# Performance work log

Measured on AMD Instinct MI355X. Metric: run time of the kernel, lower is better.

The kernel has to match this reference:

```python
import jax, jax.numpy as jnp
import numpy as np
from jax import lax

B, T, I, H = 1024, 64, 1024, 1024
EPS = 1e-5


def setup_inputs() -> dict:
    key = jax.random.key(0)
    ks = jax.random.split(key, 12)
    k = 1.0 / np.sqrt(H)  # torch RNNCell init bound
    return {
        "ui": jax.random.randint(ks[0], (B, 8), 0, 10000),
        "uv": jax.random.uniform(ks[1], (B, 8), dtype=jnp.float32),
        "ai": jax.random.randint(ks[2], (B, 8), 0, 10000),
        "av": jax.random.normal(ks[3], (B, T, I), dtype=jnp.float32),
        "y": jax.random.uniform(ks[4], (B, 1), dtype=jnp.float32),
        "W_ih": jax.random.uniform(ks[5], (H, I), minval=-k, maxval=k, dtype=jnp.float32),
        "b_ih": jax.random.uniform(ks[6], (H,), minval=-k, maxval=k, dtype=jnp.float32),
        "W_hh": jax.random.uniform(ks[7], (H, H), minval=-k, maxval=k, dtype=jnp.float32),
        "b_hh": jax.random.uniform(ks[8], (H,), minval=-k, maxval=k, dtype=jnp.float32),
        "W_out": jax.random.uniform(ks[9], (1, H), minval=-k, maxval=k, dtype=jnp.float32),
        "b_out": jax.random.uniform(ks[10], (1,), minval=-k, maxval=k, dtype=jnp.float32),
    }


def reference(ui, uv, ai, av, y, W_ih, b_ih, W_hh, b_hh, W_out, b_out):
    # av: [B, T, I] -> [T, B, I] (matches av.permute([1,0,2]) in source)
    x = jnp.transpose(av, (1, 0, 2))
    h0 = jnp.zeros((av.shape[0], W_hh.shape[0]), dtype=av.dtype)

    def step(h, xt):
        # torch.nn.RNNCell: h' = tanh(x W_ih^T + b_ih + h W_hh^T + b_hh)
        h_new = jnp.tanh(xt @ W_ih.T + b_ih + h @ W_hh.T + b_hh)
        return h_new, None

    h, _ = lax.scan(step, h0, x)
    out = jax.nn.sigmoid(h @ W_out.T + b_out)  # [B, 1]

    # y_true_bool = 1 where y >= 1e-5 else 0
    y_bool = (y >= EPS).astype(out.dtype)
    # torch BCELoss (mean reduction); clamp log like torch does (min -100)
    log_p = jnp.maximum(jnp.log(out), -100.0)
    log_1mp = jnp.maximum(jnp.log1p(-out), -100.0)
    loss = -jnp.mean(y_bool * log_p + (1.0 - y_bool) * log_1mp)
    return loss, out
```

## Files before the change

kernel.cpp:

```cpp
#include <hip/hip_runtime.h>

typedef __attribute__((ext_vector_type(8))) short bf16x8;
typedef __attribute__((ext_vector_type(4))) float f32x4;

__device__ __forceinline__ short f2bf(float f) {
    union { float f; unsigned u; } v; v.f = f;
    unsigned r = v.u + 0x7fffu + ((v.u >> 16) & 1u);
    return (short)(r >> 16);
}
__device__ __forceinline__ float bf2f(short s) {
    union { unsigned u; float f; } v; v.u = ((unsigned)(unsigned short)s) << 16;
    return v.f;
}
__device__ __forceinline__ unsigned pack2(float x, float y) {
    return (unsigned)(unsigned short)f2bf(x) | ((unsigned)(unsigned short)f2bf(y) << 16);
}
__device__ __forceinline__ uint4 pack8(float4 a, float4 b) {
    return make_uint4(pack2(a.x, a.y), pack2(a.z, a.w), pack2(b.x, b.y), pack2(b.z, b.w));
}
__device__ __forceinline__ float tanh_fast(float x) {
    float e = __expf(2.f * x);
    return 1.f - 2.f / (e + 1.f);
}

__device__ __forceinline__ void gll16(const void* gp, void* lp) {
    __builtin_amdgcn_global_load_lds(
        (__attribute__((address_space(1))) void*)gp,
        (__attribute__((address_space(3))) void*)lp, 16, 0, 0);
}

__global__ __launch_bounds__(256) void pack_w(const float* __restrict__ src,
                                              short* __restrict__ dst) {
    int idx = (blockIdx.x * 256 + threadIdx.x) * 8;
    float4 f0 = ((const float4*)(src + idx))[0];
    float4 f1 = ((const float4*)(src + idx))[1];
    *(uint4*)(dst + idx) = pack8(f0, f1);
}

__global__ void prep_b(const float* __restrict__ b_ih, const float* __restrict__ b_hh,
                       float* __restrict__ bsum) {
    int n = threadIdx.x;
    bsum[n] = b_ih[n] + b_hh[n];
}

__global__ __launch_bounds__(256) void conv_av(const float* __restrict__ av,
                                               short* __restrict__ X) {
    size_t e = ((size_t)blockIdx.x * 256 + threadIdx.x) * 8;
    size_t row = e >> 10;
    int k = (int)(e & 1023);
    int b = (int)(row >> 6), t = (int)(row & 63);
    float4 f0 = *(const float4*)(av + e);
    float4 f1 = *(const float4*)(av + e + 4);
    *(uint4*)(X + ((size_t)t * 1024 + b) * 1024 + k) = pack8(f0, f1);
}

__global__ __launch_bounds__(256) void zgemm2(const short* __restrict__ X,
                                              const short* __restrict__ Wih,
                                              const float* __restrict__ bsum,
                                              short* __restrict__ Z) {
    __shared__ short smem[16384];
    short* As = smem;
    short* Bs = smem + 8192;

    const int tid = threadIdx.x, lane = tid & 63, wave = tid >> 6;
    const int wm = wave >> 1, wn = wave & 1;
    const int m0 = blockIdx.y * 128, n0 = blockIdx.x * 128;

    const int srow = wave * 32 + (lane >> 3);
    const int scol = (lane & 7) * 8;
    const short* asrc = X   + (size_t)(m0 + srow) * 1024 + scol;
    const short* bsrc = Wih + (size_t)(n0 + srow) * 1024 + scol;
    char* aldst = (char*)As + wave * 4096;
    char* bldst = (char*)Bs + wave * 4096;

    f32x4 acc[4][4];
    #pragma unroll
    for (int i = 0; i < 4; i++)
        #pragma unroll
        for (int j = 0; j < 4; j++) acc[i][j] = (f32x4)0.0f;

    const int r = lane & 15, q = lane >> 4;
    const int koff = q * 8;

    for (int kt = 0; kt < 16; ++kt) {
        const int kbase = kt * 64;
        #pragma unroll
        for (int i = 0; i < 4; i++) {
            gll16(asrc + kbase + i * 8192, aldst + i * 1024);
            gll16(bsrc + kbase + i * 8192, bldst + i * 1024);
        }
        __syncthreads();

        #pragma unroll
        for (int ks = 0; ks < 2; ++ks) {
            bf16x8 af[4], bfr[4];
            #pragma unroll
            for (int i = 0; i < 4; i++) {
                af[i]  = *(const bf16x8*)&As[(wm * 64 + i * 16 + r) * 64 + ks * 32 + koff];
                bfr[i] = *(const bf16x8*)&Bs[(wn * 64 + i * 16 + r) * 64 + ks * 32 + koff];
            }
            #pragma unroll
            for (int i = 0; i < 4; i++)
                #pragma unroll
                for (int j = 0; j < 4; j++)
                    acc[i][j] = __builtin_amdgcn_mfma_f32_16x16x32_bf16(af[i], bfr[j], acc[i][j], 0, 0, 0);
        }
        __syncthreads();
    }

    short* Csh = smem;
    #pragma unroll
    for (int j = 0; j < 4; j++) {
        int colc = wn * 64 + j * 16 + r;
        float bs = bsum[n0 + colc];
        int chunkc = colc >> 3, rem = colc & 7;
        #pragma unroll
        for (int i = 0; i < 4; i++) {
            int rowb = wm * 64 + i * 16 + q * 4;
            #pragma unroll
            for (int rr = 0; rr < 4; rr++) {
                int row = rowb + rr;
                int sc = ((chunkc ^ (row & 7)) << 3) | rem;
                Csh[row * 128 + sc] = f2bf(acc[i][j][rr] + bs);
            }
        }
    }
    __syncthreads();
    #pragma unroll
    for (int p = 0; p < 8; p++) {
        int row = p * 16 + (tid >> 4);
        int chunk = tid & 15;
        int rc = chunk ^ (row & 7);
        uint4 v = *(const uint4*)&Csh[row * 128 + rc * 8];
        *(uint4*)(Z + (size_t)(m0 + row) * 1024 + n0 + chunk * 8) = v;
    }
}

#define ZLDK 72

__global__ __launch_bounds__(256) void zgemm(const float* __restrict__ av,
                                             const short* __restrict__ Wih,
                                             const float* __restrict__ bsum,
                                             short* __restrict__ Z) {
    __shared__ short As[128 * ZLDK];
    __shared__ short Bs[128 * ZLDK];

    const int tid = threadIdx.x, lane = tid & 63, wave = tid >> 6;
    const int wm = wave >> 1, wn = wave & 1;
    const int m0 = blockIdx.y * 128, n0 = blockIdx.x * 128;
    const int srow = tid >> 1, scol = (tid & 1) * 32;

    const int gr = m0 + srow;
    const int tt = gr >> 10, bb = gr & 1023;
    const float* asrc = av + ((size_t)bb * 64 + tt) * 1024 + scol;
    const short* bsrc = Wih + (size_t)(n0 + srow) * 1024 + scol;

    uint4 ra[4], rb[4];
    #pragma unroll
    for (int j = 0; j < 4; j++) {
        float4 f0 = *(const float4*)(asrc + 8 * j);
        float4 f1 = *(const float4*)(asrc + 8 * j + 4);
        ra[j] = pack8(f0, f1);
        rb[j] = *(const uint4*)(bsrc + 8 * j);
    }

    f32x4 acc[4][4];
    #pragma unroll
    for (int i = 0; i < 4; i++)
        #pragma unroll
        for (int j = 0; j < 4; j++) acc[i][j] = (f32x4)0.0f;

    const int r = lane & 15, q = lane >> 4;
    const int koff = q * 8;

    for (int kt = 0; kt < 16; ++kt) {
        #pragma unroll
        for (int j = 0; j < 4; j++) {
            *(uint4*)&As[srow * ZLDK + scol + 8 * j] = ra[j];
            *(uint4*)&Bs[srow * ZLDK + scol + 8 * j] = rb[j];
        }
        __syncthreads();

        if (kt < 15) {
            int k = (kt + 1) * 64;
            #pragma unroll
            for (int j = 0; j < 4; j++) {
                float4 f0 = *(const float4*)(asrc + k + 8 * j);
                float4 f1 = *(const float4*)(asrc + k + 8 * j + 4);
                ra[j] = pack8(f0, f1);
                rb[j] = *(const uint4*)(bsrc + k + 8 * j);
            }
        }

        #pragma unroll
        for (int ks = 0; ks < 2; ++ks) {
            bf16x8 af[4], bfr[4];
            #pragma unroll
            for (int i = 0; i < 4; i++) {
                af[i]  = *(const bf16x8*)&As[(wm * 64 + i * 16 + r) * ZLDK + ks * 32 + koff];
                bfr[i] = *(const bf16x8*)&Bs[(wn * 64 + i * 16 + r) * ZLDK + ks * 32 + koff];
            }
            #pragma unroll
            for (int i = 0; i < 4; i++)
                #pragma unroll
                for (int j = 0; j < 4; j++)
                    acc[i][j] = __builtin_amdgcn_mfma_f32_16x16x32_bf16(af[i], bfr[j], acc[i][j], 0, 0, 0);
        }
        __syncthreads();
    }

    #pragma unroll
    for (int j = 0; j < 4; j++) {
        int n = n0 + wn * 64 + j * 16 + r;
        float bs = bsum[n];
        #pragma unroll
        for (int i = 0; i < 4; i++) {
            int mb = m0 + wm * 64 + i * 16 + q * 4;
            #pragma unroll
            for (int rr = 0; rr < 4; rr++)
                Z[(size_t)(mb + rr) * 1024 + n] = f2bf(acc[i][j][rr] + bs);
        }
    }
}

__global__ __launch_bounds__(256) void t0_kernel(const short* __restrict__ Z,
                                                 short* __restrict__ h) {
    int idx = (blockIdx.x * 256 + threadIdx.x) * 8;
    uint4 zv = *(const uint4*)(Z + idx);
    const unsigned* zp = (const unsigned*)&zv;
    uint4 out;
    unsigned* op = (unsigned*)&out;
    #pragma unroll
    for (int j = 0; j < 4; j++) {
        float lo = tanh_fast(bf2f((short)(zp[j] & 0xffffu)));
        float hi = tanh_fast(bf2f((short)(zp[j] >> 16)));
        op[j] = pack2(lo, hi);
    }
    *(uint4*)(h + idx) = out;
}

#define SLDK 136

__global__ __launch_bounds__(512) void step_kernel(const short* __restrict__ Whh,
                                                   const short* __restrict__ Z,
                                                   const short* __restrict__ h_in,
                                                   short* __restrict__ h_out, int t) {
    __shared__ short As[64 * SLDK];
    __shared__ short Bs[64 * SLDK];

    const int tid = threadIdx.x, lane = tid & 63, wave = tid >> 6;
    const int wm = wave >> 2, wn = wave & 3;
    const int m0 = blockIdx.y * 64, n0 = blockIdx.x * 64;
    const int srow = tid >> 3, scol = (tid & 7) * 16;

    const short* asrc = h_in + (size_t)(m0 + srow) * 1024 + scol;
    const short* bsrc = Whh + (size_t)(n0 + srow) * 1024 + scol;

    uint4 ra0 = *(const uint4*)asrc;
    uint4 ra1 = *(const uint4*)(asrc + 8);
    uint4 rb0 = *(const uint4*)bsrc;
    uint4 rb1 = *(const uint4*)(bsrc + 8);

    f32x4 acc[2];
    acc[0] = (f32x4)0.0f;
    acc[1] = (f32x4)0.0f;

    const int r = lane & 15, q = lane >> 4;
    const int arow = wm * 32 + r, brow = wn * 16 + r;
    const int koff = q * 8;

    for (int chunk = 0; chunk < 8; ++chunk) {
        *(uint4*)&As[srow * SLDK + scol]     = ra0;
        *(uint4*)&As[srow * SLDK + scol + 8] = ra1;
        *(uint4*)&Bs[srow * SLDK + scol]     = rb0;
        *(uint4*)&Bs[srow * SLDK + scol + 8] = rb1;
        __syncthreads();

        if (chunk < 7) {
            int k = (chunk + 1) * 128;
            ra0 = *(const uint4*)(asrc + k);
            ra1 = *(const uint4*)(asrc + k + 8);
            rb0 = *(const uint4*)(bsrc + k);
            rb1 = *(const uint4*)(bsrc + k + 8);
        }

        #pragma unroll
        for (int ks = 0; ks < 4; ++ks) {
            bf16x8 a0 = *(const bf16x8*)&As[arow * SLDK + ks * 32 + koff];
            bf16x8 a1 = *(const bf16x8*)&As[(arow + 16) * SLDK + ks * 32 + koff];
            bf16x8 b  = *(const bf16x8*)&Bs[brow * SLDK + ks * 32 + koff];
            acc[0] = __builtin_amdgcn_mfma_f32_16x16x32_bf16(a0, b, acc[0], 0, 0, 0);
            acc[1] = __builtin_amdgcn_mfma_f32_16x16x32_bf16(a1, b, acc[1], 0, 0, 0);
        }
        __syncthreads();
    }

    const short* zt = Z + ((size_t)t << 20);
    int n = n0 + wn * 16 + r;
    #pragma unroll
    for (int mi = 0; mi < 2; mi++) {
        int mb = m0 + wm * 32 + mi * 16 + q * 4;
        #pragma unroll
        for (int rr = 0; rr < 4; rr++) {
            float z = bf2f(zt[((size_t)(mb + rr) << 10) + n]);
            h_out[((size_t)(mb + rr) << 10) + n] = f2bf(tanh_fast(acc[mi][rr] + z));
        }
    }
}

__global__ __launch_bounds__(256) void head_kernel(const short* __restrict__ h,
                                                   const float* __restrict__ W_out,
                                                   const float* __restrict__ b_out,
                                                   float* __restrict__ p) {
    int b    = blockIdx.x * 4 + (threadIdx.x >> 6);
    int lane = threadIdx.x & 63;
    float s = 0.f;
    for (int k = lane; k < 1024; k += 64)
        s += bf2f(h[(size_t)b * 1024 + k]) * W_out[k];
    #pragma unroll
    for (int off = 32; off > 0; off >>= 1) s += __shfl_down(s, off);
    if (lane == 0) p[b] = 1.f / (1.f + __expf(-(s + b_out[0])));
}

__global__ __launch_bounds__(1024) void loss_kernel(const float* __restrict__ p,
                                                    const float* __restrict__ y,
                                                    float* __restrict__ loss) {
    __shared__ float red[1024];
    int b = threadIdx.x;
    float pv = p[b];
    float yb = (y[b] >= 1e-5f) ? 1.f : 0.f;
    float lp = fmaxf(logf(pv), -100.f);
    float l1 = fmaxf(log1pf(-pv), -100.f);
    red[b] = yb * lp + (1.f - yb) * l1;
    __syncthreads();
    for (int s = 512; s > 0; s >>= 1) {
        if (b < s) red[b] += red[b + s];
        __syncthreads();
    }
    if (b == 0) loss[0] = -red[0] / 1024.f;
}

extern "C" void kernel_launch(void* const* d_in, const int* in_sizes, int n_in,
                              void* d_out, int out_size, void* d_ws, size_t ws_size,
                              hipStream_t stream) {
    const float* av    = (const float*)d_in[3];
    const float* y     = (const float*)d_in[4];
    const float* W_ih  = (const float*)d_in[5];
    const float* b_ih  = (const float*)d_in[6];
    const float* W_hh  = (const float*)d_in[7];
    const float* b_hh  = (const float*)d_in[8];
    const float* W_out = (const float*)d_in[9];
    const float* b_out = (const float*)d_in[10];
    float* out = (float*)d_out;

    char* ws = (char*)d_ws;
    short* Wih_bf = (short*)ws;
    short* Whh_bf = (short*)(ws + (2u << 20));
    float* bsum   = (float*)(ws + (4u << 20));
    short* hb0    = (short*)(ws + (5u << 20));
    short* hb1    = (short*)(ws + (7u << 20));
    short* Z      = (short*)(ws + (9u << 20));
    short* X      = (short*)(ws + (137u << 20));

    pack_w<<<512, 256, 0, stream>>>(W_ih, Wih_bf);
    pack_w<<<512, 256, 0, stream>>>(W_hh, Whh_bf);
    prep_b<<<1, 1024, 0, stream>>>(b_ih, b_hh, bsum);

    if (ws_size >= ((size_t)266 << 20)) {
        conv_av<<<32768, 256, 0, stream>>>(av, X);
        zgemm2<<<dim3(8, 512), 256, 0, stream>>>(X, Wih_bf, bsum, Z);
    } else {
        zgemm<<<dim3(8, 512), 256, 0, stream>>>(av, Wih_bf, bsum, Z);
    }

    short* hbuf[2] = { hb0, hb1 };
    t0_kernel<<<512, 256, 0, stream>>>(Z, hb1);
    for (int t = 1; t < 64; ++t) {
        short* hin  = hbuf[t & 1];
        short* hout = hbuf[(t + 1) & 1];
        step_kernel<<<dim3(16, 16), 512, 0, stream>>>(Whh_bf, Z, hin, hout, t);
    }
    head_kernel<<<256, 256, 0, stream>>>(hb0, W_out, b_out, out + 1);
    loss_kernel<<<1, 1024, 0, stream>>>(out + 1, y, out);
}
```

Baseline: 1.272 ms.

## Add double-buffered swizzled recurrent step kernel and remap zgemm tiles

Adds a new recurrent step kernel that streams h and W_hh tiles straight into XOR-swizzled LDS with global_load_lds, double-buffers the K loop, prefetches the Z tile into shared memory, and writes h through a shared staging buffer as coalesced 16-byte stores. The input-projection GEMM gets the same XOR swizzle to avoid LDS bank conflicts, and a 1D block index remapped to group tiles for L2 reuse. The goal is to cut stall and bank-conflict time in the 63 serial step launches and in the large GEMM. It costs more LDS per block and adds indexing complexity. The new path runs only when the workspace is large enough.

```diff
diff --git a/kernel.cpp b/kernel.cpp
--- a/kernel.cpp
+++ b/kernel.cpp
@@ -21,6 +21,18 @@
 __device__ __forceinline__ float tanh_fast(float x) {
     float e = __expf(2.f * x);
     return 1.f - 2.f / (e + 1.f);
+}
+__device__ __forceinline__ uint4 tanh8(uint4 zv) {
+    const unsigned* zp = (const unsigned*)&zv;
+    uint4 out;
+    unsigned* op = (unsigned*)&out;
+    #pragma unroll
+    for (int j = 0; j < 4; j++) {
+        float lo = tanh_fast(bf2f((short)(zp[j] & 0xffffu)));
+        float hi = tanh_fast(bf2f((short)(zp[j] >> 16)));
+        op[j] = pack2(lo, hi);
+    }
+    return out;
 }
 
 __device__ __forceinline__ void gll16(const void* gp, void* lp) {
@@ -64,10 +76,14 @@
 
     const int tid = threadIdx.x, lane = tid & 63, wave = tid >> 6;
     const int wm = wave >> 1, wn = wave & 1;
-    const int m0 = blockIdx.y * 128, n0 = blockIdx.x * 128;
+    const int pid = blockIdx.x;
+    const int slot = pid >> 3;
+    const int mt = (pid & 7) * 64 + (slot >> 3);
+    const int nt = slot & 7;
+    const int m0 = mt * 128, n0 = nt * 128;
 
     const int srow = wave * 32 + (lane >> 3);
-    const int scol = (lane & 7) * 8;
+    const int scol = ((lane & 7) ^ (lane >> 3)) * 8;
     const short* asrc = X   + (size_t)(m0 + srow) * 1024 + scol;
     const short* bsrc = Wih + (size_t)(n0 + srow) * 1024 + scol;
     char* aldst = (char*)As + wave * 4096;
@@ -80,7 +96,6 @@
         for (int j = 0; j < 4; j++) acc[i][j] = (f32x4)0.0f;
 
     const int r = lane & 15, q = lane >> 4;
-    const int koff = q * 8;
 
     for (int kt = 0; kt < 16; ++kt) {
         const int kbase = kt * 64;
@@ -96,8 +111,10 @@
             bf16x8 af[4], bfr[4];
             #pragma unroll
             for (int i = 0; i < 4; i++) {
-                af[i]  = *(const bf16x8*)&As[(wm * 64 + i * 16 + r) * 64 + ks * 32 + koff];
-                bfr[i] = *(const bf16x8*)&Bs[(wn * 64 + i * 16 + r) * 64 + ks * 32 + koff];
+                int ar = wm * 64 + i * 16 + r;
+                int br = wn * 64 + i * 16 + r;
+                af[i]  = *(const bf16x8*)&As[ar * 64 + (((ks * 4 + q) ^ (r & 7)) << 3)];
+                bfr[i] = *(const bf16x8*)&Bs[br * 64 + (((ks * 4 + q) ^ (r & 7)) << 3)];
             }
             #pragma unroll
             for (int i = 0; i < 4; i++)
@@ -226,17 +243,7 @@
 __global__ __launch_bounds__(256) void t0_kernel(const short* __restrict__ Z,
                                                  short* __restrict__ h) {
     int idx = (blockIdx.x * 256 + threadIdx.x) * 8;
-    uint4 zv = *(const uint4*)(Z + idx);
-    const unsigned* zp = (const unsigned*)&zv;
-    uint4 out;
-    unsigned* op = (unsigned*)&out;
-    #pragma unroll
-    for (int j = 0; j < 4; j++) {
-        float lo = tanh_fast(bf2f((short)(zp[j] & 0xffffu)));
-        float hi = tanh_fast(bf2f((short)(zp[j] >> 16)));
-        op[j] = pack2(lo, hi);
-    }
-    *(uint4*)(h + idx) = out;
+    *(uint4*)(h + idx) = tanh8(*(const uint4*)(Z + idx));
 }
 
 #define SLDK 136
@@ -305,6 +312,91 @@
             float z = bf2f(zt[((size_t)(mb + rr) << 10) + n]);
             h_out[((size_t)(mb + rr) << 10) + n] = f2bf(tanh_fast(acc[mi][rr] + z));
         }
+    }
+}
+
+__global__ __launch_bounds__(512) void step3(const short* __restrict__ Whh,
+                                             const short* __restrict__ Z,
+                                             const short* __restrict__ h_in,
+                                             short* __restrict__ h_out, int t) {
+    __shared__ short As[2][64 * 128];
+    __shared__ short Bs[2][64 * 128];
+    __shared__ short Zs[64 * 64];
+
+    const int tid = threadIdx.x, lane = tid & 63, wave = tid >> 6;
+    const int wm = wave >> 2, wn = wave & 3;
+    const int pid = blockIdx.x;
+    const int bx = ((pid & 7) << 1) | ((pid >> 3) & 1);
+    const int by = pid >> 4;
+    const int m0 = by * 64, n0 = bx * 64;
+    const int r = lane & 15, q = lane >> 4;
+
+    const int c16 = lane & 15;
+    const int R0 = wave * 4 + (lane >> 4);
+    const int sw0 = (c16 ^ (R0 & 7)) << 3;
+    const int sw1 = (c16 ^ ((R0 & 7))) << 3;
+
+    const short* abase = h_in + (size_t)(m0 + R0) * 1024;
+    const short* bbase = Whh  + (size_t)(n0 + R0) * 1024;
+
+    gll16(abase + sw0,                 (char*)&As[0][0] + (wave * 4) * 256);
+    gll16(abase + 32 * 1024 + sw1,     (char*)&As[0][0] + (32 + wave * 4) * 256);
+    gll16(bbase + sw0,                 (char*)&Bs[0][0] + (wave * 4) * 256);
+    gll16(bbase + 32 * 1024 + sw1,     (char*)&Bs[0][0] + (32 + wave * 4) * 256);
+    {
+        int zr = wave * 8 + (lane >> 3);
+        gll16(Z + ((size_t)t << 20) + (size_t)(m0 + zr) * 1024 + n0 + ((lane & 7) << 3),
+              (char*)Zs + wave * 1024);
+    }
+    __syncthreads();
+
+    f32x4 acc0 = (f32x4)0.0f, acc1 = (f32x4)0.0f;
+    const int arow0 = (wm * 32 + r) * 128;
+    const int arow1 = (wm * 32 + 16 + r) * 128;
+    const int brow  = (wn * 16 + r) * 128;
+    const int axor  = r & 7;
+
+    for (int kt = 0; kt < 8; ++kt) {
+        const int cur = kt & 1;
+        if (kt < 7) {
+            const int nk = (kt + 1) * 128;
+            const int nb = cur ^ 1;
+            gll16(abase + nk + sw0,             (char*)&As[nb][0] + (wave * 4) * 256);
+            gll16(abase + 32 * 1024 + nk + sw1, (char*)&As[nb][0] + (32 + wave * 4) * 256);
+            gll16(bbase + nk + sw0,             (char*)&Bs[nb][0] + (wave * 4) * 256);
+            gll16(bbase + 32 * 1024 + nk + sw1, (char*)&Bs[nb][0] + (32 + wave * 4) * 256);
+        }
+        #pragma unroll
+        for (int ks = 0; ks < 4; ++ks) {
+            const int co = (((ks * 4 + q) ^ axor) << 3);
+            bf16x8 a0 = *(const bf16x8*)&As[cur][arow0 + co];
+            bf16x8 a1 = *(const bf16x8*)&As[cur][arow1 + co];
+            bf16x8 b  = *(const bf16x8*)&Bs[cur][brow + co];
+            acc0 = __builtin_amdgcn_mfma_f32_16x16x32_bf16(a0, b, acc0, 0, 0, 0);
+            acc1 = __builtin_amdgcn_mfma_f32_16x16x32_bf16(a1, b, acc1, 0, 0, 0);
+        }
+        __syncthreads();
+    }
+
+    short* Csh = &As[0][0];
+    const int col = wn * 16 + r;
+    const int cc = col >> 3, rem = col & 7;
+    #pragma unroll
+    for (int mi = 0; mi < 2; mi++) {
+        const f32x4 a = mi ? acc1 : acc0;
+        #pragma unroll
+        for (int rr = 0; rr < 4; rr++) {
+            int row = wm * 32 + mi * 16 + q * 4 + rr;
+            float z = bf2f(Zs[row * 64 + col]);
+            Csh[row * 64 + ((cc ^ (row & 7)) << 3) + rem] = f2bf(tanh_fast(a[rr] + z));
+        }
+    }
+    __syncthreads();
+    {
+        int orow = tid >> 3, ochunk = tid & 7;
+        int orc = ochunk ^ (orow & 7);
+        uint4 v = *(const uint4*)&Csh[orow * 64 + orc * 8];
+        *(uint4*)(h_out + (size_t)(m0 + orow) * 1024 + n0 + ochunk * 8) = v;
     }
 }
 
@@ -366,20 +458,22 @@
     pack_w<<<512, 256, 0, stream>>>(W_hh, Whh_bf);
     prep_b<<<1, 1024, 0, stream>>>(b_ih, b_hh, bsum);
 
-    if (ws_size >= ((size_t)266 << 20)) {
+    bool bigws = ws_size >= ((size_t)266 << 20);
+
+    short* hbuf[2] = { hb0, hb1 };
+    if (bigws) {
         conv_av<<<32768, 256, 0, stream>>>(av, X);
-        zgemm2<<<dim3(8, 512), 256, 0, stream>>>(X, Wih_bf, bsum, Z);
+        zgemm2<<<4096, 256, 0, stream>>>(X, Wih_bf, bsum, Z);
+        t0_kernel<<<512, 256, 0, stream>>>(Z, hb1);
+        for (int t = 1; t < 64; ++t)
+            step3<<<256, 512, 0, stream>>>(Whh_bf, Z, hbuf[t & 1], hbuf[(t + 1) & 1], t);
     } else {
         zgemm<<<dim3(8, 512), 256, 0, stream>>>(av, Wih_bf, bsum, Z);
-    }
-
-    short* hbuf[2] = { hb0, hb1 };
-    t0_kernel<<<512, 256, 0, stream>>>(Z, hb1);
-    for (int t = 1; t < 64; ++t) {
-        short* hin  = hbuf[t & 1];
-        short* hout = hbuf[(t + 1) & 1];
-        step_kernel<<<dim3(16, 16), 512, 0, stream>>>(Whh_bf, Z, hin, hout, t);
-    }
+        t0_kernel<<<512, 256, 0, stream>>>(Z, hb1);
+        for (int t = 1; t < 64; ++t)
+            step_kernel<<<dim3(16, 16), 512, 0, stream>>>(Whh_bf, Z, hbuf[t & 1], hbuf[(t + 1) & 1], t);
+    }
+
     head_kernel<<<256, 256, 0, stream>>>(hb0, W_out, b_out, out + 1);
     loss_kernel<<<1, 1024, 0, stream>>>(out + 1, y, out);
 }
```

Measured after the change: 1.255 ms. Within noise of the previous version (-1.3%).
